# Kernel tuning notes

Measured on AMD Instinct MI355X. Metric: run time of the kernel, lower is better.

The kernel has to match this reference:

```python
import jax, jax.numpy as jnp
import numpy as np

DIM = 1024
HEADS = 16
DIM_HEAD = 64
CHUNK = 64
INNER = HEADS * DIM_HEAD  # 1024


def setup_inputs() -> dict:
    key = jax.random.key(0)
    k1, k2, k3 = jax.random.split(key, 3)
    x = jax.random.normal(k1, (4, 4096, DIM), dtype=jnp.float32)
    # nn.Linear weights stored as (out, in); apply as x @ W.T
    w_qkv = jax.random.normal(k2, (INNER * 3, DIM), dtype=jnp.float32) * (DIM ** -0.5)
    w_out = jax.random.normal(k3, (DIM, INNER), dtype=jnp.float32) * (INNER ** -0.5)
    b_out = jnp.zeros((DIM,), dtype=jnp.float32)
    return {"x": x, "w_qkv": w_qkv, "w_out": w_out, "b_out": b_out}


def reference(x, w_qkv, w_out, b_out):
    b, n, _ = x.shape
    scale = DIM_HEAD ** -0.5
    qkv = jnp.einsum('bnd,ed->bne', x, w_qkv)  # (b, n, 3*inner)
    q, k, v = jnp.split(qkv, 3, axis=-1)
    nblk = n // CHUNK

    def to_blocks(t):
        # (b, n, h*d) -> (b, h, nblk, c, d)
        t = t.reshape(b, n, HEADS, DIM_HEAD).transpose(0, 2, 1, 3)
        return t.reshape(b, HEADS, nblk, CHUNK, DIM_HEAD)

    qb, kb, vb = to_blocks(q), to_blocks(k), to_blocks(v)
    scores = jnp.einsum('bhgqd,bhgkd->bhgqk', qb, kb) * scale  # block-local
    attn = jax.nn.softmax(scores, axis=-1)
    ob = jnp.einsum('bhgqk,bhgkd->bhgqd', attn, vb)
    out = ob.reshape(b, HEADS, n, DIM_HEAD).transpose(0, 2, 1, 3).reshape(b, n, INNER)
    return jnp.einsum('bne,de->bnd', out, w_out) + b_out
```

## Files before the change

### kernel.cpp

```cpp
#include <hip/hip_runtime.h>
#include <stdint.h>

typedef __attribute__((ext_vector_type(8))) short bf16x8;
typedef __attribute__((ext_vector_type(4))) float f32x4;

__device__ __forceinline__ unsigned short bf16_of(float f) {
  union { float f; uint32_t u; } x; x.f = f;
  uint32_t r = x.u + 0x7fffu + ((x.u >> 16) & 1u);
  return (unsigned short)(r >> 16);
}

#define GLD16(gp, lp) __builtin_amdgcn_global_load_lds( \
    (const __attribute__((address_space(1))) uint32_t*)(gp), \
    (__attribute__((address_space(3))) uint32_t*)(lp), 16, 0, 0)

#define BAR() do { asm volatile("" ::: "memory"); __builtin_amdgcn_s_barrier(); asm volatile("" ::: "memory"); } while (0)

__global__ void cvt_f32_bf16(const float* __restrict__ src,
                             unsigned short* __restrict__ dst, int n4) {
  int i = blockIdx.x * blockDim.x + threadIdx.x;
  int stride = gridDim.x * blockDim.x;
  for (int j = i; j < n4; j += stride) {
    float4 f = ((const float4*)src)[j];
    union { unsigned short s[4]; uint2 v; } u;
    u.s[0] = bf16_of(f.x); u.s[1] = bf16_of(f.y);
    u.s[2] = bf16_of(f.z); u.s[3] = bf16_of(f.w);
    ((uint2*)dst)[j] = u.v;
  }
}

template<int BIAS, int OUTF32>
__global__ __launch_bounds__(512, 2)
void gemm256(const unsigned short* __restrict__ A,
             const unsigned short* __restrict__ B,
             void* __restrict__ C, const float* __restrict__ bias,
             int M, int N, int K)
{
  __shared__ __align__(1024) unsigned short sm[65536];
  char* const smb = (char*)sm;
  const int tid = threadIdx.x, w = tid >> 6, lane = tid & 63;
  const int wm = w >> 2, wn = w & 3;
  const int fr = lane & 15, kg = lane >> 4;
  const int swz = (fr & 7) << 4;
  const int srow = lane >> 3, sslot = lane & 7;

  const int nbx = N >> 8;
  const int nwg = gridDim.x;
  const int bid = blockIdx.x;
  const int bid2 = (bid & 7) * (nwg >> 3) + (bid >> 3);
  const int bm0 = (bid2 / nbx) << 8;
  const int bn0 = (bid2 % nbx) << 8;
  const int NT = K >> 6;

  f32x4 acc[8][4] = {};

  auto STAGE = [&](int buf, int opnd, int half, int kt) {
    const unsigned short* G = opnd ? B : A;
    const int grow0 = opnd ? bn0 : bm0;
    char* region = smb + opnd * 65536 + buf * 32768 + half * 16384;
    const int k0 = kt << 6;
    #pragma unroll
    for (int i = 0; i < 2; ++i) {
      const int c = i * 8 + w;
      const int row = half * 128 + c * 8 + srow;
      const int slot = sslot ^ srow;
      GLD16(G + (size_t)(grow0 + row) * K + k0 + slot * 8, region + c * 1024);
    }
  };
  auto LDA = [&](char* Ab, int j, int ks) -> bf16x8 {
    const int r = 32 * j + 16 * wm + fr;
    return *(const bf16x8*)(Ab + r * 128 + ((ks * 64 + kg * 16) ^ swz));
  };
  auto LDB = [&](char* Bb, int l, int ks) -> bf16x8 {
    const int r = 64 * l + 16 * wn + fr;
    return *(const bf16x8*)(Bb + r * 128 + ((ks * 64 + kg * 16) ^ swz));
  };

  STAGE(0, 0, 0, 0);
  STAGE(0, 1, 1, 0);
  STAGE(0, 0, 1, 0);
  STAGE(0, 1, 0, 0);
  if (NT > 1) {
    STAGE(1, 0, 0, 1);
    STAGE(1, 1, 1, 1);
    asm volatile("s_waitcnt vmcnt(4)" ::: "memory");
  } else {
    asm volatile("s_waitcnt vmcnt(0)" ::: "memory");
  }
  BAR();

  for (int t = 0; t < NT; ++t) {
    char* Ab = smb + (t & 1) * 32768;
    char* Bb = smb + 65536 + (t & 1) * 32768;
    bf16x8 a[4][2], b[2][2];

    #pragma unroll
    for (int j = 0; j < 4; ++j) { a[j][0] = LDA(Ab, j, 0); a[j][1] = LDA(Ab, j, 1); }
    #pragma unroll
    for (int l = 0; l < 2; ++l) { b[l][0] = LDB(Bb, l, 0); b[l][1] = LDB(Bb, l, 1); }
    if (t + 1 < NT) STAGE((t + 1) & 1, 0, 1, t + 1);
    BAR();
    __builtin_amdgcn_s_setprio(1);
    #pragma unroll
    for (int j = 0; j < 4; ++j)
      #pragma unroll
      for (int l = 0; l < 2; ++l) {
        acc[j][l] = __builtin_amdgcn_mfma_f32_16x16x32_bf16(a[j][0], b[l][0], acc[j][l], 0, 0, 0);
        acc[j][l] = __builtin_amdgcn_mfma_f32_16x16x32_bf16(a[j][1], b[l][1], acc[j][l], 0, 0, 0);
      }
    __builtin_amdgcn_s_setprio(0);
    BAR();

    #pragma unroll
    for (int l = 0; l < 2; ++l) { b[l][0] = LDB(Bb, l + 2, 0); b[l][1] = LDB(Bb, l + 2, 1); }
    if (t + 1 < NT) STAGE((t + 1) & 1, 1, 0, t + 1);
    BAR();
    __builtin_amdgcn_s_setprio(1);
    #pragma unroll
    for (int j = 0; j < 4; ++j)
      #pragma unroll
      for (int l = 0; l < 2; ++l) {
        acc[j][l + 2] = __builtin_amdgcn_mfma_f32_16x16x32_bf16(a[j][0], b[l][0], acc[j][l + 2], 0, 0, 0);
        acc[j][l + 2] = __builtin_amdgcn_mfma_f32_16x16x32_bf16(a[j][1], b[l][1], acc[j][l + 2], 0, 0, 0);
      }
    __builtin_amdgcn_s_setprio(0);
    BAR();

    #pragma unroll
    for (int j = 0; j < 4; ++j) { a[j][0] = LDA(Ab, j + 4, 0); a[j][1] = LDA(Ab, j + 4, 1); }
    if (t + 2 < NT) STAGE(t & 1, 0, 0, t + 2);
    BAR();
    __builtin_amdgcn_s_setprio(1);
    #pragma unroll
    for (int j = 0; j < 4; ++j)
      #pragma unroll
      for (int l = 0; l < 2; ++l) {
        acc[j + 4][l + 2] = __builtin_amdgcn_mfma_f32_16x16x32_bf16(a[j][0], b[l][0], acc[j + 4][l + 2], 0, 0, 0);
        acc[j + 4][l + 2] = __builtin_amdgcn_mfma_f32_16x16x32_bf16(a[j][1], b[l][1], acc[j + 4][l + 2], 0, 0, 0);
      }
    __builtin_amdgcn_s_setprio(0);
    BAR();

    #pragma unroll
    for (int l = 0; l < 2; ++l) { b[l][0] = LDB(Bb, l, 0); b[l][1] = LDB(Bb, l, 1); }
    if (t + 2 < NT) STAGE(t & 1, 1, 1, t + 2);
    BAR();
    __builtin_amdgcn_s_setprio(1);
    #pragma unroll
    for (int j = 0; j < 4; ++j)
      #pragma unroll
      for (int l = 0; l < 2; ++l) {
        acc[j + 4][l] = __builtin_amdgcn_mfma_f32_16x16x32_bf16(a[j][0], b[l][0], acc[j + 4][l], 0, 0, 0);
        acc[j + 4][l] = __builtin_amdgcn_mfma_f32_16x16x32_bf16(a[j][1], b[l][1], acc[j + 4][l], 0, 0, 0);
      }
    __builtin_amdgcn_s_setprio(0);
    if (t + 2 < NT) { asm volatile("s_waitcnt vmcnt(4)" ::: "memory"); }
    else            { asm volatile("s_waitcnt vmcnt(0)" ::: "memory"); }
    BAR();
  }

  #pragma unroll
  for (int l = 0; l < 4; ++l) {
    const int col = bn0 + 64 * l + 16 * wn + fr;
    float bb = 0.0f;
    if (BIAS && OUTF32) bb = bias[col];
    #pragma unroll
    for (int j = 0; j < 8; ++j) {
      const int row0 = bm0 + 32 * j + 16 * wm + kg * 4;
      #pragma unroll
      for (int rr = 0; rr < 4; ++rr) {
        if (OUTF32)
          ((float*)C)[(size_t)(row0 + rr) * N + col] = acc[j][l][rr] + bb;
        else
          ((unsigned short*)C)[(size_t)(row0 + rr) * N + col] = bf16_of(acc[j][l][rr]);
      }
    }
  }
}

__global__ __launch_bounds__(256, 2)
void attn_block(const unsigned short* __restrict__ qkv,
                unsigned short* __restrict__ o)
{
  __shared__ __align__(1024) unsigned short Qs[64 * 64];
  __shared__ __align__(1024) unsigned short Ks[64 * 64];
  __shared__ __align__(1024) unsigned short Vt[64 * 64];
  __shared__ __align__(1024) unsigned short Ps[64 * 64];
  const int tid = threadIdx.x, w = tid >> 6, lane = tid & 63;
  const int g = blockIdx.x, h = blockIdx.y, b = blockIdx.z;
  const size_t mbase = (size_t)b * 4096 + (size_t)g * 64;
  const unsigned short* qg = qkv + mbase * 3072 + h * 64;
  const unsigned short* kgl = qkv + mbase * 3072 + 1024 + h * 64;
  const unsigned short* vg = qkv + mbase * 3072 + 2048 + h * 64;

  #pragma unroll
  for (int i = 0; i < 2; ++i) {
    const int chunk = i * 4 + w;
    const int row = chunk * 8 + (lane >> 3);
    const int c8 = (lane & 7) ^ (row & 7);
    GLD16(qg + (size_t)row * 3072 + c8 * 8, (char*)Qs + chunk * 1024);
    GLD16(kgl + (size_t)row * 3072 + c8 * 8, (char*)Ks + chunk * 1024);
  }
  #pragma unroll
  for (int i = 0; i < 2; ++i) {
    const int c = i * 256 + tid;
    const int n = c >> 3, d0 = (c & 7) * 8;
    bf16x8 v = *(const bf16x8*)(vg + (size_t)n * 3072 + d0);
    #pragma unroll
    for (int j = 0; j < 8; ++j) {
      const int d = d0 + j;
      const int bo = d * 128 + n * 2;
      *(unsigned short*)((char*)Vt + (bo ^ ((d & 7) << 4))) = (unsigned short)v[j];
    }
  }
  __syncthreads();

  const int fr = lane & 15, kg = lane >> 4;
  f32x4 s[4] = {};
  #pragma unroll
  for (int kt = 0; kt < 2; ++kt) {
    const int kb = kt * 64 + kg * 16;
    const int rq = w * 16 + fr;
    bf16x8 aq = *(const bf16x8*)((const char*)Qs + rq * 128 + (kb ^ ((rq & 7) << 4)));
    #pragma unroll
    for (int nf = 0; nf < 4; ++nf) {
      const int rk = nf * 16 + fr;
      bf16x8 bk = *(const bf16x8*)((const char*)Ks + rk * 128 + (kb ^ ((rk & 7) << 4)));
      s[nf] = __builtin_amdgcn_mfma_f32_16x16x32_bf16(aq, bk, s[nf], 0, 0, 0);
    }
  }

  const float scale = 0.125f;
  float inv[4];
  #pragma unroll
  for (int r = 0; r < 4; ++r) {
    float m0 = fmaxf(fmaxf(s[0][r], s[1][r]), fmaxf(s[2][r], s[3][r]));
    #pragma unroll
    for (int d = 1; d < 16; d <<= 1) m0 = fmaxf(m0, __shfl_xor(m0, d));
    float sum = 0.0f;
    #pragma unroll
    for (int nf = 0; nf < 4; ++nf) {
      float p = __expf((s[nf][r] - m0) * scale);
      s[nf][r] = p;
      sum += p;
    }
    #pragma unroll
    for (int d = 1; d < 16; d <<= 1) sum += __shfl_xor(sum, d);
    inv[r] = 1.0f / sum;
  }

  #pragma unroll
  for (int r = 0; r < 4; ++r) {
    const int m = w * 16 + kg * 4 + r;
    #pragma unroll
    for (int nf = 0; nf < 4; ++nf) {
      const int bo = m * 128 + (nf * 16 + fr) * 2;
      *(unsigned short*)((char*)Ps + (bo ^ ((m & 7) << 4))) = bf16_of(s[nf][r] * inv[r]);
    }
  }
  __syncthreads();

  f32x4 oa[4] = {};
  #pragma unroll
  for (int kt = 0; kt < 2; ++kt) {
    const int kb = kt * 64 + kg * 16;
    const int rp = w * 16 + fr;
    bf16x8 ap = *(const bf16x8*)((const char*)Ps + rp * 128 + (kb ^ ((rp & 7) << 4)));
    #pragma unroll
    for (int df = 0; df < 4; ++df) {
      const int rv = df * 16 + fr;
      bf16x8 bv = *(const bf16x8*)((const char*)Vt + rv * 128 + (kb ^ ((rv & 7) << 4)));
      oa[df] = __builtin_amdgcn_mfma_f32_16x16x32_bf16(ap, bv, oa[df], 0, 0, 0);
    }
  }
  #pragma unroll
  for (int df = 0; df < 4; ++df) {
    #pragma unroll
    for (int r = 0; r < 4; ++r) {
      const size_t row = mbase + w * 16 + kg * 4 + r;
      const int col = h * 64 + df * 16 + fr;
      o[row * 1024 + col] = bf16_of(oa[df][r]);
    }
  }
}

extern "C" void kernel_launch(void* const* d_in, const int* in_sizes, int n_in,
                              void* d_out, int out_size, void* d_ws, size_t ws_size,
                              hipStream_t stream) {
  const float* x     = (const float*)d_in[0];
  const float* w_qkv = (const float*)d_in[1];
  const float* w_out = (const float*)d_in[2];
  const float* b_out = (const float*)d_in[3];
  char* ws = (char*)d_ws;
  const size_t SZ_X  = (size_t)16384 * 1024 * 2;
  const size_t SZ_WQ = (size_t)3072 * 1024 * 2;
  const size_t SZ_WO = (size_t)1024 * 1024 * 2;
  unsigned short* xb  = (unsigned short*)ws;
  unsigned short* wqb = (unsigned short*)(ws + SZ_X);
  unsigned short* wob = (unsigned short*)(ws + SZ_X + SZ_WQ);
  unsigned short* qkv = (unsigned short*)(ws + SZ_X + SZ_WQ + SZ_WO);
  unsigned short* ob  = xb;

  cvt_f32_bf16<<<2048, 256, 0, stream>>>(x, xb, 16384 * 1024 / 4);
  cvt_f32_bf16<<<512, 256, 0, stream>>>(w_qkv, wqb, 3072 * 1024 / 4);
  cvt_f32_bf16<<<256, 256, 0, stream>>>(w_out, wob, 1024 * 1024 / 4);
  gemm256<0,0><<<dim3(768), 512, 0, stream>>>(xb, wqb, qkv, nullptr, 16384, 3072, 1024);
  attn_block<<<dim3(64, 16, 4), 256, 0, stream>>>(qkv, ob);
  gemm256<1,1><<<dim3(256), 512, 0, stream>>>(ob, wob, d_out, b_out, 16384, 1024, 1024);
}
```

Measured before the change: 212.8 us.

## Make GEMM persistent across tiles with cross-tile prefetch and grouped XCD mapping

Turns the 256x256 GEMM into a persistent kernel. Each of 256 workgroups processes NSEG output tiles in sequence, and the load pipeline keeps prefetching across tile boundaries so the next tile's K-slices arrive while the current tile's epilogue runs. It also reorders tile assignment into column groups of width GW per XCD to improve L2 reuse, and changes the stage ordering and waitcnt depth. The cost is a more complex schedule and a fixed assumption that K is 1024 (16 k-steps) and that the grid exactly covers the tile count.

```diff
diff --git a/kernel.cpp b/kernel.cpp
--- a/kernel.cpp
+++ b/kernel.cpp
@@ -29,12 +29,12 @@
   }
 }
 
-template<int BIAS, int OUTF32>
+template<int BIAS, int OUTF32, int GW, int NSEG>
 __global__ __launch_bounds__(512, 2)
-void gemm256(const unsigned short* __restrict__ A,
-             const unsigned short* __restrict__ B,
-             void* __restrict__ C, const float* __restrict__ bias,
-             int M, int N, int K)
+void gemm256p(const unsigned short* __restrict__ A,
+              const unsigned short* __restrict__ B,
+              void* __restrict__ C, const float* __restrict__ bias,
+              int N, int K)
 {
   __shared__ __align__(1024) unsigned short sm[65536];
   char* const smb = (char*)sm;
@@ -43,28 +43,27 @@
   const int fr = lane & 15, kg = lane >> 4;
   const int swz = (fr & 7) << 4;
   const int srow = lane >> 3, sslot = lane & 7;
-
-  const int nbx = N >> 8;
-  const int nwg = gridDim.x;
-  const int bid = blockIdx.x;
-  const int bid2 = (bid & 7) * (nwg >> 3) + (bid >> 3);
-  const int bm0 = (bid2 / nbx) << 8;
-  const int bn0 = (bid2 % nbx) << 8;
-  const int NT = K >> 6;
-
-  f32x4 acc[8][4] = {};
-
-  auto STAGE = [&](int buf, int opnd, int half, int kt) {
-    const unsigned short* G = opnd ? B : A;
-    const int grow0 = opnd ? bn0 : bm0;
-    char* region = smb + opnd * 65536 + buf * 32768 + half * 16384;
-    const int k0 = kt << 6;
-    #pragma unroll
-    for (int i = 0; i < 2; ++i) {
-      const int c = i * 8 + w;
+  const int cXcd = blockIdx.x & 7, iIdx = blockIdx.x >> 3;
+  const int NT_tot = NSEG * 16;
+
+  auto tileMN = [&](int s, int& mt, int& nt) {
+    const int T = cXcd * (32 * NSEG) + s * 32 + iIdx;
+    const int g = T / (64 * GW), rr = T % (64 * GW);
+    mt = rr / GW; nt = g * GW + rr % GW;
+  };
+
+  auto STAGE = [&](int u, int opnd, int half) {
+    int mt, nt; tileMN(u >> 4, mt, nt);
+    const unsigned short* G_ = opnd ? B : A;
+    const int grow0 = (opnd ? nt : mt) << 8;
+    char* region = smb + opnd * 65536 + (u & 1) * 32768 + half * 16384;
+    const int k0 = (u & 15) << 6;
+    #pragma unroll
+    for (int i2 = 0; i2 < 2; ++i2) {
+      const int c = i2 * 8 + w;
       const int row = half * 128 + c * 8 + srow;
       const int slot = sslot ^ srow;
-      GLD16(G + (size_t)(grow0 + row) * K + k0 + slot * 8, region + c * 1024);
+      GLD16(G_ + (size_t)(grow0 + row) * K + k0 + slot * 8, region + c * 1024);
     }
   };
   auto LDA = [&](char* Ab, int j, int ks) -> bf16x8 {
@@ -76,105 +75,107 @@
     return *(const bf16x8*)(Bb + r * 128 + ((ks * 64 + kg * 16) ^ swz));
   };
 
-  STAGE(0, 0, 0, 0);
-  STAGE(0, 1, 1, 0);
-  STAGE(0, 0, 1, 0);
-  STAGE(0, 1, 0, 0);
-  if (NT > 1) {
-    STAGE(1, 0, 0, 1);
-    STAGE(1, 1, 1, 1);
-    asm volatile("s_waitcnt vmcnt(4)" ::: "memory");
-  } else {
-    asm volatile("s_waitcnt vmcnt(0)" ::: "memory");
-  }
+  f32x4 acc[8][4] = {};
+
+  STAGE(0, 0, 0); STAGE(0, 1, 0); STAGE(0, 0, 1); STAGE(0, 1, 1);
+  STAGE(1, 0, 0); STAGE(1, 1, 1); STAGE(1, 0, 1);
+  asm volatile("s_waitcnt vmcnt(6)" ::: "memory");
   BAR();
 
-  for (int t = 0; t < NT; ++t) {
-    char* Ab = smb + (t & 1) * 32768;
-    char* Bb = smb + 65536 + (t & 1) * 32768;
-    bf16x8 a[4][2], b[2][2];
-
-    #pragma unroll
-    for (int j = 0; j < 4; ++j) { a[j][0] = LDA(Ab, j, 0); a[j][1] = LDA(Ab, j, 1); }
-    #pragma unroll
-    for (int l = 0; l < 2; ++l) { b[l][0] = LDB(Bb, l, 0); b[l][1] = LDB(Bb, l, 1); }
-    if (t + 1 < NT) STAGE((t + 1) & 1, 0, 1, t + 1);
-    BAR();
-    __builtin_amdgcn_s_setprio(1);
-    #pragma unroll
-    for (int j = 0; j < 4; ++j)
-      #pragma unroll
-      for (int l = 0; l < 2; ++l) {
-        acc[j][l] = __builtin_amdgcn_mfma_f32_16x16x32_bf16(a[j][0], b[l][0], acc[j][l], 0, 0, 0);
-        acc[j][l] = __builtin_amdgcn_mfma_f32_16x16x32_bf16(a[j][1], b[l][1], acc[j][l], 0, 0, 0);
+  for (int s = 0; s < NSEG; ++s) {
+    for (int tt = 0; tt < 16; ++tt) {
+      const int G = s * 16 + tt;
+      char* Ab = smb + (G & 1) * 32768;
+      char* Bb = smb + 65536 + (G & 1) * 32768;
+      bf16x8 a[4][2], b[2][2], b0[2][2];
+
+      #pragma unroll
+      for (int j = 0; j < 4; ++j) { a[j][0] = LDA(Ab, j, 0); a[j][1] = LDA(Ab, j, 1); }
+      #pragma unroll
+      for (int l = 0; l < 2; ++l) { b0[l][0] = LDB(Bb, l, 0); b0[l][1] = LDB(Bb, l, 1); }
+      if (G + 1 < NT_tot) STAGE(G + 1, 1, 0);
+      BAR();
+      __builtin_amdgcn_s_setprio(1);
+      #pragma unroll
+      for (int j = 0; j < 4; ++j)
+        #pragma unroll
+        for (int l = 0; l < 2; ++l) {
+          acc[j][l] = __builtin_amdgcn_mfma_f32_16x16x32_bf16(a[j][0], b0[l][0], acc[j][l], 0, 0, 0);
+          acc[j][l] = __builtin_amdgcn_mfma_f32_16x16x32_bf16(a[j][1], b0[l][1], acc[j][l], 0, 0, 0);
+        }
+      __builtin_amdgcn_s_setprio(0);
+      BAR();
+
+      #pragma unroll
+      for (int l = 0; l < 2; ++l) { b[l][0] = LDB(Bb, l + 2, 0); b[l][1] = LDB(Bb, l + 2, 1); }
+      if (G + 2 < NT_tot) STAGE(G + 2, 0, 0);
+      BAR();
+      __builtin_amdgcn_s_setprio(1);
+      #pragma unroll
+      for (int j = 0; j < 4; ++j)
+        #pragma unroll
+        for (int l = 0; l < 2; ++l) {
+          acc[j][l + 2] = __builtin_amdgcn_mfma_f32_16x16x32_bf16(a[j][0], b[l][0], acc[j][l + 2], 0, 0, 0);
+          acc[j][l + 2] = __builtin_amdgcn_mfma_f32_16x16x32_bf16(a[j][1], b[l][1], acc[j][l + 2], 0, 0, 0);
+        }
+      __builtin_amdgcn_s_setprio(0);
+      BAR();
+
+      #pragma unroll
+      for (int j = 0; j < 4; ++j) { a[j][0] = LDA(Ab, j + 4, 0); a[j][1] = LDA(Ab, j + 4, 1); }
+      if (G + 2 < NT_tot) STAGE(G + 2, 1, 1);
+      BAR();
+      __builtin_amdgcn_s_setprio(1);
+      #pragma unroll
+      for (int j = 0; j < 4; ++j)
+        #pragma unroll
+        for (int l = 0; l < 2; ++l) {
+          acc[j + 4][l + 2] = __builtin_amdgcn_mfma_f32_16x16x32_bf16(a[j][0], b[l][0], acc[j + 4][l + 2], 0, 0, 0);
+          acc[j + 4][l + 2] = __builtin_amdgcn_mfma_f32_16x16x32_bf16(a[j][1], b[l][1], acc[j + 4][l + 2], 0, 0, 0);
+        }
+      __builtin_amdgcn_s_setprio(0);
+      BAR();
+
+      if (G + 2 < NT_tot) STAGE(G + 2, 0, 1);
+      BAR();
+      __builtin_amdgcn_s_setprio(1);
+      #pragma unroll
+      for (int j = 0; j < 4; ++j)
+        #pragma unroll
+        for (int l = 0; l < 2; ++l) {
+          acc[j + 4][l] = __builtin_amdgcn_mfma_f32_16x16x32_bf16(a[j][0], b0[l][0], acc[j + 4][l], 0, 0, 0);
+          acc[j + 4][l] = __builtin_amdgcn_mfma_f32_16x16x32_bf16(a[j][1], b0[l][1], acc[j + 4][l], 0, 0, 0);
+        }
+      __builtin_amdgcn_s_setprio(0);
+      if (G == NT_tot - 2)      { asm volatile("s_waitcnt vmcnt(0)" ::: "memory"); }
+      else if (G < NT_tot - 2)  { asm volatile("s_waitcnt vmcnt(6)" ::: "memory"); }
+      BAR();
+    }
+
+    int mt, nt; tileMN(s, mt, nt);
+    const int bm0 = mt << 8, bn0 = nt << 8;
+    #pragma unroll
+    for (int l = 0; l < 4; ++l) {
+      const int col = bn0 + 64 * l + 16 * wn + fr;
+      float bb = 0.0f;
+      if (BIAS && OUTF32) bb = bias[col];
+      #pragma unroll
+      for (int j = 0; j < 8; ++j) {
+        const int row0 = bm0 + 32 * j + 16 * wm + kg * 4;
+        #pragma unroll
+        for (int rr = 0; rr < 4; ++rr) {
+          if (OUTF32)
+            ((float*)C)[(size_t)(row0 + rr) * N + col] = acc[j][l][rr] + bb;
+          else
+            ((unsigned short*)C)[(size_t)(row0 + rr) * N + col] = bf16_of(acc[j][l][rr]);
+        }
       }
-    __builtin_amdgcn_s_setprio(0);
-    BAR();
-
-    #pragma unroll
-    for (int l = 0; l < 2; ++l) { b[l][0] = LDB(Bb, l + 2, 0); b[l][1] = LDB(Bb, l + 2, 1); }
-    if (t + 1 < NT) STAGE((t + 1) & 1, 1, 0, t + 1);
-    BAR();
-    __builtin_amdgcn_s_setprio(1);
-    #pragma unroll
-    for (int j = 0; j < 4; ++j)
-      #pragma unroll
-      for (int l = 0; l < 2; ++l) {
-        acc[j][l + 2] = __builtin_amdgcn_mfma_f32_16x16x32_bf16(a[j][0], b[l][0], acc[j][l + 2], 0, 0, 0);
-        acc[j][l + 2] = __builtin_amdgcn_mfma_f32_16x16x32_bf16(a[j][1], b[l][1], acc[j][l + 2], 0, 0, 0);
-      }
-    __builtin_amdgcn_s_setprio(0);
-    BAR();
-
-    #pragma unroll
-    for (int j = 0; j < 4; ++j) { a[j][0] = LDA(Ab, j + 4, 0); a[j][1] = LDA(Ab, j + 4, 1); }
-    if (t + 2 < NT) STAGE(t & 1, 0, 0, t + 2);
-    BAR();
-    __builtin_amdgcn_s_setprio(1);
-    #pragma unroll
-    for (int j = 0; j < 4; ++j)
-      #pragma unroll
-      for (int l = 0; l < 2; ++l) {
-        acc[j + 4][l + 2] = __builtin_amdgcn_mfma_f32_16x16x32_bf16(a[j][0], b[l][0], acc[j + 4][l + 2], 0, 0, 0);
-        acc[j + 4][l + 2] = __builtin_amdgcn_mfma_f32_16x16x32_bf16(a[j][1], b[l][1], acc[j + 4][l + 2], 0, 0, 0);
-      }
-    __builtin_amdgcn_s_setprio(0);
-    BAR();
-
-    #pragma unroll
-    for (int l = 0; l < 2; ++l) { b[l][0] = LDB(Bb, l, 0); b[l][1] = LDB(Bb, l, 1); }
-    if (t + 2 < NT) STAGE(t & 1, 1, 1, t + 2);
-    BAR();
-    __builtin_amdgcn_s_setprio(1);
-    #pragma unroll
-    for (int j = 0; j < 4; ++j)
-      #pragma unroll
-      for (int l = 0; l < 2; ++l) {
-        acc[j + 4][l] = __builtin_amdgcn_mfma_f32_16x16x32_bf16(a[j][0], b[l][0], acc[j + 4][l], 0, 0, 0);
-        acc[j + 4][l] = __builtin_amdgcn_mfma_f32_16x16x32_bf16(a[j][1], b[l][1], acc[j + 4][l], 0, 0, 0);
-      }
-    __builtin_amdgcn_s_setprio(0);
-    if (t + 2 < NT) { asm volatile("s_waitcnt vmcnt(4)" ::: "memory"); }
-    else            { asm volatile("s_waitcnt vmcnt(0)" ::: "memory"); }
-    BAR();
-  }
-
-  #pragma unroll
-  for (int l = 0; l < 4; ++l) {
-    const int col = bn0 + 64 * l + 16 * wn + fr;
-    float bb = 0.0f;
-    if (BIAS && OUTF32) bb = bias[col];
-    #pragma unroll
-    for (int j = 0; j < 8; ++j) {
-      const int row0 = bm0 + 32 * j + 16 * wm + kg * 4;
-      #pragma unroll
-      for (int rr = 0; rr < 4; ++rr) {
-        if (OUTF32)
-          ((float*)C)[(size_t)(row0 + rr) * N + col] = acc[j][l][rr] + bb;
-        else
-          ((unsigned short*)C)[(size_t)(row0 + rr) * N + col] = bf16_of(acc[j][l][rr]);
-      }
-    }
+    }
+    #pragma unroll
+    for (int j = 0; j < 8; ++j)
+      #pragma unroll
+      for (int l = 0; l < 4; ++l)
+        acc[j][l] = f32x4{0.f, 0.f, 0.f, 0.f};
   }
 }
 
@@ -304,7 +305,7 @@
   cvt_f32_bf16<<<2048, 256, 0, stream>>>(x, xb, 16384 * 1024 / 4);
   cvt_f32_bf16<<<512, 256, 0, stream>>>(w_qkv, wqb, 3072 * 1024 / 4);
   cvt_f32_bf16<<<256, 256, 0, stream>>>(w_out, wob, 1024 * 1024 / 4);
-  gemm256<0,0><<<dim3(768), 512, 0, stream>>>(xb, wqb, qkv, nullptr, 16384, 3072, 1024);
+  gemm256p<0,0,6,3><<<dim3(256), 512, 0, stream>>>(xb, wqb, qkv, nullptr, 3072, 1024);
   attn_block<<<dim3(64, 16, 4), 256, 0, stream>>>(qkv, ob);
-  gemm256<1,1><<<dim3(256), 512, 0, stream>>>(ob, wob, d_out, b_out, 16384, 1024, 1024);
-}
+  gemm256p<1,1,4,1><<<dim3(256), 512, 0, stream>>>(ob, wob, d_out, b_out, 1024, 1024);
+}
```

Result: faster. 197.6 us (-7.1%).
